# Kernel optimization log

Measured on AMD Instinct MI355X. Metric: run time of the kernel, lower is better.

## Reference

```python
import jax, jax.numpy as jnp
import numpy as np

B, N, D, H = 2, 2048, 1024, 16
Dh = D // H
SCALE = Dh ** -0.5


def setup_inputs() -> dict:
    key = jax.random.key(0)
    ks = jax.random.split(key, 5)
    init = lambda k, sh, fan: (jax.random.normal(k, sh, jnp.float32) / np.sqrt(fan)).astype(jnp.float32)
    return {
        "x": jax.random.normal(ks[0], (B, N, D), jnp.float32),
        "w_qkv": init(ks[1], (D, 3 * D), D),   # to_qkv (no bias)
        "w_hkv": init(ks[2], (D, 2 * D), D),   # hkv_processor: Linear(dim, 2*dim), split -> HK, HV
        "w_out": init(ks[3], (D, D), D),       # to_out weight
        "b_out": jnp.zeros((D,), jnp.float32), # to_out bias
        "alpha": jnp.ones((1, H, 1, 1), jnp.float32),
    }


def _split_heads(t):  # (B,N,D) -> (B,H,N,Dh)
    return t.reshape(B, N, H, Dh).transpose(0, 2, 1, 3)


def _rope(x, theta=10000.0):
    # lucidrains rotary_embedding_torch: interleaved pairs (x[2i], x[2i+1])
    n, dh = x.shape[-2], x.shape[-1]
    freqs = 1.0 / (theta ** (jnp.arange(0, dh, 2, dtype=jnp.float32) / dh))
    ang = jnp.arange(n, dtype=jnp.float32)[:, None] * freqs          # (N, Dh/2)
    cos = jnp.repeat(jnp.cos(ang), 2, axis=-1)                        # (N, Dh)
    sin = jnp.repeat(jnp.sin(ang), 2, axis=-1)
    xp = x.reshape(*x.shape[:-1], dh // 2, 2)
    xrot = jnp.stack((-xp[..., 1], xp[..., 0]), axis=-1).reshape(x.shape)
    return x * cos + xrot * sin


def reference(x, w_qkv, w_hkv, w_out, b_out, alpha):
    q, k, v = (_split_heads(t) for t in jnp.split(x @ w_qkv, 3, axis=-1))
    hk, hv = (_split_heads(t) for t in jnp.split(x @ w_hkv, 2, axis=-1))
    q = _rope(q)
    k = _rope(k)

    qk = jnp.einsum('bhnd,bhmd->bhnm', q, k) * SCALE          # (B,H,N,N)
    hkk = jnp.einsum('bhnd,bhmd->bhnm', hk, k)                # (B,H,N,N)
    qhk = jnp.sum(q * hk, axis=-1, keepdims=True)             # (B,H,N,1)
    scores = qk - jax.nn.silu(hkk * qhk * SCALE)

    mask = jnp.tril(jnp.ones((N, N), dtype=bool))
    scores = jnp.where(mask, scores, -jnp.inf)
    W = jax.nn.softmax(scores, axis=-1)

    hvv = jnp.einsum('bhnd,bhmd->bhnm', hv, v)                # (B,H,N,N)
    mod = jnp.sum(hvv * W, axis=-1, keepdims=True)            # (B,H,N,1)
    o = jnp.einsum('bhnm,bhmd->bhnd', W, v) - jax.nn.sigmoid(alpha) * mod * hv

    attn_out = o.transpose(0, 2, 1, 3).reshape(B, N, D)
    return attn_out @ w_out + b_out
```

## Files before the change

kernel.cpp:

```cpp
#include <hip/hip_runtime.h>
#include <math.h>

typedef unsigned int u32;
typedef unsigned short u16;
typedef __attribute__((ext_vector_type(4))) float f32x4;
typedef __attribute__((ext_vector_type(8))) short s16x8;

#define BB 2
#define NN 2048
#define DD 1024
#define HH 16
#define ROWS 4096
#define QC 5120
#define SCALE 0.125f
#define LOG2E 1.44269504088896f
#define SC2 (SCALE * LOG2E)
#define DEFER_THR 8.0f

#if __has_builtin(__builtin_amdgcn_exp2f)
#define EXP2(x) __builtin_amdgcn_exp2f(x)
#else
#define EXP2(x) __expf((x) * 0.69314718056f)
#endif
#if __has_builtin(__builtin_amdgcn_rcpf)
#define RCP(x) __builtin_amdgcn_rcpf(x)
#else
#define RCP(x) (1.0f / (x))
#endif

__device__ __forceinline__ u16 f2bf(float x) {
    u32 u = __float_as_uint(x);
    return (u16)((u + 0x7FFFu + ((u >> 16) & 1u)) >> 16);
}
__device__ __forceinline__ float bf2f(u16 h) {
    return __uint_as_float(((u32)h) << 16);
}
__device__ __forceinline__ u32 cvtpk(float lo, float hi) {
    u32 r;
    asm("v_cvt_pk_bf16_f32 %0, %1, %2" : "=v"(r) : "v"(lo), "v"(hi));
    return r;
}
__device__ __forceinline__ void gload16(const void* g, void* l) {
    __builtin_amdgcn_global_load_lds(
        (const __attribute__((address_space(1))) unsigned int*)g,
        (__attribute__((address_space(3))) unsigned int*)l, 16, 0, 0);
}

__device__ __forceinline__ void vt_write(char* vbb, uint4 vreg, int srow, int sch)
{
    uint4 oth;
    oth.x = (u32)__shfl_xor((int)vreg.x, 8); oth.y = (u32)__shfl_xor((int)vreg.y, 8);
    oth.z = (u32)__shfl_xor((int)vreg.z, 8); oth.w = (u32)__shfl_xor((int)vreg.w, 8);
    const bool odd = (srow & 1);
    u32 ma = odd ? vreg.z : vreg.x, mb = odd ? vreg.w : vreg.y;
    u32 oa = odd ? oth.z : oth.x,  ob = odd ? oth.w : oth.y;
    u32 ea = odd ? oa : ma, eb = odd ? ob : mb;
    u32 da = odd ? ma : oa, db = odd ? mb : ob;
    u32 pk0 = (ea & 0xffffu) | (da << 16);
    u32 pk1 = (ea >> 16)     | (da & 0xffff0000u);
    u32 pk2 = (eb & 0xffffu) | (db << 16);
    u32 pk3 = (eb >> 16)     | (db & 0xffff0000u);
    const int s = srow >> 1;
    const int d0 = sch * 8 + (odd ? 4 : 0);
    const int sb = (s & 3) * 4;
    *(u32*)(vbb + (d0 + 0) * 128 + ((((s >> 2) ^ ((d0 + 0) & 7) ^ sch) << 4)) + sb) = pk0;
    *(u32*)(vbb + (d0 + 1) * 128 + ((((s >> 2) ^ ((d0 + 1) & 7) ^ sch) << 4)) + sb) = pk1;
    *(u32*)(vbb + (d0 + 2) * 128 + ((((s >> 2) ^ ((d0 + 2) & 7) ^ sch) << 4)) + sb) = pk2;
    *(u32*)(vbb + (d0 + 3) * 128 + ((((s >> 2) ^ ((d0 + 3) & 7) ^ sch) << 4)) + sb) = pk3;
}

__global__ __launch_bounds__(256) void prep(const float* __restrict__ x,
                                            const float* __restrict__ wqkv,
                                            const float* __restrict__ whkv,
                                            const float* __restrict__ wout,
                                            uint4* __restrict__ xb,
                                            u16* __restrict__ wT,
                                            float* __restrict__ tab)
{
    __shared__ float T[64][65];
    const int bid = blockIdx.x;
    if (bid < 2048) {
        int t = bid * 256 + threadIdx.x;
        const float4 a = ((const float4*)x)[2 * t];
        const float4 b = ((const float4*)x)[2 * t + 1];
        uint4 o;
        o.x = f2bf(a.x) | ((u32)f2bf(a.y) << 16);
        o.y = f2bf(a.z) | ((u32)f2bf(a.w) << 16);
        o.z = f2bf(b.x) | ((u32)f2bf(b.y) << 16);
        o.w = f2bf(b.z) | ((u32)f2bf(b.w) << 16);
        xb[t] = o;
    } else if (bid < 3584) {
        const int idx = bid - 2048;
        const int bc = idx % 96;
        const int k0 = (idx / 96) * 64;
        const int c0 = bc * 64;
        const float* src; int stride; int csrc;
        if (bc < 48)      { src = wqkv; stride = 3072; csrc = c0; }
        else if (bc < 80) { src = whkv; stride = 2048; csrc = c0 - 3072; }
        else              { src = wout; stride = 1024; csrc = c0 - 5120; }
        const int t = threadIdx.x;
        const int r = t >> 4, c4 = t & 15;
#pragma unroll
        for (int i = 0; i < 4; ++i) {
            int kk = r + 16 * i;
            float4 v = *(const float4*)&src[(size_t)(k0 + kk) * stride + csrc + 4 * c4];
            T[kk][4 * c4 + 0] = v.x; T[kk][4 * c4 + 1] = v.y;
            T[kk][4 * c4 + 2] = v.z; T[kk][4 * c4 + 3] = v.w;
        }
        __syncthreads();
#pragma unroll
        for (int i = 0; i < 4; ++i) {
            int cc = r + 16 * i;
            u32 lo = f2bf(T[4 * c4 + 0][cc]) | ((u32)f2bf(T[4 * c4 + 1][cc]) << 16);
            u32 hi = f2bf(T[4 * c4 + 2][cc]) | ((u32)f2bf(T[4 * c4 + 3][cc]) << 16);
            *(uint2*)&wT[(size_t)(c0 + cc) * 1024 + k0 + 4 * c4] = make_uint2(lo, hi);
        }
    } else {
        int t = (bid - 3584) * 256 + threadIdx.x;
        int n = t >> 6, col = t & 63, i = col & 31;
        float ang = (float)n * exp2f(-(float)i * 0.41524101186092029f);
        tab[t] = (col < 32) ? cosf(ang) : sinf(ang);
    }
}

template <int BF16_OUT>
__global__ __launch_bounds__(256, 2) void gemm_bf16(
    const u16* __restrict__ A, int lda,
    const u16* __restrict__ B, int ldb,
    void* __restrict__ C, int ldc,
    const float* __restrict__ bias, const float* __restrict__ tab, int K)
{
    __shared__ u16 As[128 * 64];
    __shared__ u16 Bs[128 * 64];
    const int tid = threadIdx.x;
    const int lane = tid & 63, w = tid >> 6;
    const int g = lane >> 4, c = lane & 15;
    const int wr = w >> 1, wc = w & 1;
    const int rb0 = blockIdx.y * 128, cb0 = blockIdx.x * 128;

    f32x4 acc[4][4];
#pragma unroll
    for (int i = 0; i < 4; ++i)
#pragma unroll
        for (int j = 0; j < 4; ++j) {
            acc[i][j][0] = 0.f; acc[i][j][1] = 0.f; acc[i][j][2] = 0.f; acc[i][j][3] = 0.f;
        }

    const int srow = tid >> 3, sch = tid & 7;
    const int scol = ((sch ^ (srow & 7)) * 8);
    const u16* asrc = A + (size_t)(rb0 + srow) * lda + scol;
    const u16* bsrc = B + (size_t)(cb0 + srow) * ldb + scol;

    for (int k0 = 0; k0 < K; k0 += 64) {
        __syncthreads();
#pragma unroll
        for (int r = 0; r < 4; ++r) {
            gload16(asrc + (size_t)(32 * r) * lda + k0, (char*)As + r * 4096 + w * 1024);
            gload16(bsrc + (size_t)(32 * r) * ldb + k0, (char*)Bs + r * 4096 + w * 1024);
        }
        __syncthreads();
#pragma unroll
        for (int kk = 0; kk < 2; ++kk) {
            s16x8 a[4], b[4];
#pragma unroll
            for (int rb = 0; rb < 4; ++rb) {
                int row = wr * 64 + rb * 16 + c;
                a[rb] = *(const s16x8*)((const char*)As + row * 128 + ((((kk << 2) + g) ^ (row & 7)) << 4));
            }
#pragma unroll
            for (int cb = 0; cb < 4; ++cb) {
                int row = wc * 64 + cb * 16 + c;
                b[cb] = *(const s16x8*)((const char*)Bs + row * 128 + ((((kk << 2) + g) ^ (row & 7)) << 4));
            }
#pragma unroll
            for (int rb = 0; rb < 4; ++rb)
#pragma unroll
                for (int cb = 0; cb < 4; ++cb)
                    acc[rb][cb] = __builtin_amdgcn_mfma_f32_16x16x32_bf16(a[rb], b[cb], acc[rb][cb], 0, 0, 0);
        }
    }

    if (BF16_OUT && tab && cb0 >= 1024 && cb0 < 2048) {
#pragma unroll
        for (int rb = 0; rb < 4; ++rb)
#pragma unroll
            for (int cb = 0; cb < 4; ++cb) {
                const int i = ((wc * 64 + cb * 16 + c) & 63) >> 1;
#pragma unroll
                for (int e = 0; e < 4; ++e) {
                    int n = (rb0 + wr * 64 + rb * 16 + g * 4 + e) & (NN - 1);
                    float co = tab[(n << 6) + i], si = tab[(n << 6) + 32 + i];
                    float self = acc[rb][cb][e];
                    float part = __shfl_xor(self, 1);
                    acc[rb][cb][e] = (c & 1) ? fmaf(self, co, part * si)
                                             : fmaf(self, co, -part * si);
                }
            }
    }

#pragma unroll
    for (int rb = 0; rb < 4; ++rb) {
#pragma unroll
        for (int cb = 0; cb < 4; ++cb) {
            if (BF16_OUT) {
                uint2 keep = make_uint2(0, 0);
#pragma unroll
                for (int e = 0; e < 4; ++e) {
                    u32 me = f2bf(acc[rb][cb][e]);
                    u32 x1 = (u32)__shfl_xor((int)me, 1);
                    u32 pair = (c & 1) ? ((x1 & 0xffffu) | (me << 16)) : ((me & 0xffffu) | (x1 << 16));
                    u32 x2 = (u32)__shfl_xor((int)pair, 2);
                    u32 q0 = (c & 2) ? x2 : pair;
                    u32 q1 = (c & 2) ? pair : x2;
                    if ((c & 3) == e) keep = make_uint2(q0, q1);
                }
                int row = rb0 + wr * 64 + rb * 16 + g * 4 + (c & 3);
                int col = cb0 + wc * 64 + cb * 16 + (c & ~3);
                *(uint2*)((u16*)C + (size_t)row * ldc + col) = keep;
            } else {
                int col = cb0 + wc * 64 + cb * 16 + c;
                float bv = bias ? bias[col] : 0.f;
#pragma unroll
                for (int e = 0; e < 4; ++e) {
                    int row = rb0 + wr * 64 + rb * 16 + g * 4 + e;
                    ((float*)C)[(size_t)row * ldc + col] = acc[rb][cb][e] + bv;
                }
            }
        }
    }
}

__global__ __launch_bounds__(256, 4) void attn(
    const u16* __restrict__ qkvh, const float* __restrict__ alpha,
    const float* __restrict__ tab, u16* __restrict__ aout)
{
    __shared__ u16 Kb[2][64 * 64];
    __shared__ u16 Vt[2][64 * 64];

    const int bid = blockIdx.x;
    const int j = bid >> 5;
    const int qt = (j < 8) ? (31 - j) : (j < 16) ? (j + 8) : (j < 24) ? (31 - j) : (j - 24);
    const int bh = 4 * (bid & 7) + ((bid >> 3) & 3);
    const int b = bh >> 4, h = bh & 15;
    const int tid = threadIdx.x;
    const int w = tid >> 6, lane = tid & 63;
    const int g = lane >> 4, c = lane & 15;
    const u16* base = qkvh + (size_t)b * NN * QC;
    const int q0 = qt * 64;
    const int nrow = q0 + w * 16 + c;

    const int srow = tid >> 3, sch = tid & 7;
    const int kscol = (sch ^ ((srow & 3) | (((srow >> 3) & 1) << 2))) * 8;
    const u16* ksrc0 = base + (size_t)srow * QC + 1024 + h * 64 + kscol;
    const u16* vsrc0 = base + (size_t)srow * QC + 2048 + h * 64 + sch * 8;

    const float sig_a = RCP(1.f + EXP2(-alpha[h] * LOG2E));
    const int cbase = (8 * (c >> 2) + (c & 3)) * 128;

    gload16(ksrc0, (char*)&Kb[0][0] + w * 1024);
    gload16(ksrc0 + (size_t)32 * QC, (char*)&Kb[0][0] + 4096 + w * 1024);
    uint4 vr0 = *(const uint4*)vsrc0;
    uint4 vr1 = *(const uint4*)(vsrc0 + (size_t)32 * QC);
    vt_write((char*)&Vt[0][0], vr0, srow, sch);
    vt_write((char*)&Vt[0][0], vr1, srow + 32, sch);

    s16x8 qf[2], hf[2];
    float qhL;
    {
        const u16* qp_ = base + (size_t)nrow * QC + h * 64;
        float accq = 0.f;
#pragma unroll
        for (int kk = 0; kk < 2; ++kk) {
            uint4 qv = *(const uint4*)(qp_ + ((kk * 4 + g) * 8));
            uint4 hv = *(const uint4*)(qp_ + 3072 + ((kk * 4 + g) * 8));
            const u16* qe = (const u16*)&qv;
            const u16* he = (const u16*)&hv;
            u32 ow[4];
#pragma unroll
            for (int m2 = 0; m2 < 4; ++m2) {
                int i = (kk * 4 + g) * 4 + m2;
                float co = tab[(nrow << 6) + i], si = tab[(nrow << 6) + 32 + i];
                float x0 = bf2f(qe[2 * m2]), x1 = bf2f(qe[2 * m2 + 1]);
                float r0 = x0 * co - x1 * si;
                float r1 = x1 * co + x0 * si;
                accq += r0 * bf2f(he[2 * m2]) + r1 * bf2f(he[2 * m2 + 1]);
                ow[m2] = (u32)f2bf(r0) | ((u32)f2bf(r1) << 16);
            }
            union { s16x8 v; u32 u[4]; } uq, uh;
            uq.u[0] = ow[0]; uq.u[1] = ow[1]; uq.u[2] = ow[2]; uq.u[3] = ow[3];
            uh.u[0] = hv.x; uh.u[1] = hv.y; uh.u[2] = hv.z; uh.u[3] = hv.w;
            qf[kk] = uq.v; hf[kk] = uh.v;
        }
        accq += __shfl_xor(accq, 16);
        accq += __shfl_xor(accq, 32);
        qhL = accq * SC2;
    }
    __syncthreads();

    f32x4 y[4];
#pragma unroll
    for (int db = 0; db < 4; ++db) { y[db][0] = 0.f; y[db][1] = 0.f; y[db][2] = 0.f; y[db][3] = 0.f; }
    float m = -INFINITY, l = 0.f;

    for (int kt = 0; kt <= qt; ++kt) {
        const int cur = kt & 1;
        const bool haveNext = (kt < qt);
        uint4 vr0n, vr1n;
        if (haveNext) {
            gload16(ksrc0 + (size_t)((kt + 1) * 64) * QC, (char*)&Kb[cur ^ 1][0] + w * 1024);
            gload16(ksrc0 + (size_t)((kt + 1) * 64 + 32) * QC, (char*)&Kb[cur ^ 1][0] + 4096 + w * 1024);
            vr0n = *(const uint4*)(vsrc0 + (size_t)((kt + 1) * 64) * QC);
            vr1n = *(const uint4*)(vsrc0 + (size_t)((kt + 1) * 64 + 32) * QC);
        }

        f32x4 sq[4], sh4[4];
#pragma unroll
        for (int kb = 0; kb < 4; ++kb) {
            sq[kb][0] = 0.f; sq[kb][1] = 0.f; sq[kb][2] = 0.f; sq[kb][3] = 0.f;
            sh4[kb][0] = 0.f; sh4[kb][1] = 0.f; sh4[kb][2] = 0.f; sh4[kb][3] = 0.f;
        }
        const char* kbp = (const char*)&Kb[cur][0] + cbase;
        __builtin_amdgcn_s_setprio(1);
#pragma unroll
        for (int kb = 0; kb < 4; ++kb) {
#pragma unroll
            for (int kk = 0; kk < 2; ++kk) {
                s16x8 kf = *(const s16x8*)(kbp + (kb & 1) * 512 + (kb >> 1) * 4096 +
                                           ((((kk << 2) + g) ^ (c & 7)) << 4));
                sq[kb] = __builtin_amdgcn_mfma_f32_16x16x32_bf16(kf, qf[kk], sq[kb], 0, 0, 0);
                sh4[kb] = __builtin_amdgcn_mfma_f32_16x16x32_bf16(kf, hf[kk], sh4[kb], 0, 0, 0);
            }
        }
        __builtin_amdgcn_s_setprio(0);
        const bool needmask = (kt == qt);
        float mx = -INFINITY;
#pragma unroll
        for (int kb = 0; kb < 4; ++kb) {
#pragma unroll
            for (int e = 0; e < 4; ++e) {
                float zp = sh4[kb][e] * qhL;
                float sil = zp * RCP(1.f + EXP2(-zp));
                float s = fmaf(sq[kb][e], SC2, -sil);
                if (needmask) {
                    int kg = kt * 64 + 32 * (kb >> 1) + 8 * g + 4 * (kb & 1) + e;
                    if (kg > nrow) s = -INFINITY;
                }
                sq[kb][e] = s;
                mx = fmaxf(mx, s);
            }
        }
        mx = fmaxf(mx, __shfl_xor(mx, 16));
        mx = fmaxf(mx, __shfl_xor(mx, 32));
        if (!__all(mx <= m + DEFER_THR)) {
            const float mnew = fmaxf(m, mx);
            const float scl = EXP2(m - mnew);
            m = mnew;
            l *= scl;
#pragma unroll
            for (int db = 0; db < 4; ++db) {
                y[db][0] *= scl; y[db][1] *= scl; y[db][2] *= scl; y[db][3] *= scl;
            }
        }
        float rs = 0.f;
#pragma unroll
        for (int kb = 0; kb < 4; ++kb)
#pragma unroll
            for (int e = 0; e < 4; ++e) {
                float p = EXP2(sq[kb][e] - m);
                sq[kb][e] = p;
                rs += p;
            }
        rs += __shfl_xor(rs, 16);
        rs += __shfl_xor(rs, 32);
        l += rs;
        union { s16x8 v; u32 u[4]; } pa[2];
#pragma unroll
        for (int kk = 0; kk < 2; ++kk) {
            pa[kk].u[0] = cvtpk(sq[2 * kk][0], sq[2 * kk][1]);
            pa[kk].u[1] = cvtpk(sq[2 * kk][2], sq[2 * kk][3]);
            pa[kk].u[2] = cvtpk(sq[2 * kk + 1][0], sq[2 * kk + 1][1]);
            pa[kk].u[3] = cvtpk(sq[2 * kk + 1][2], sq[2 * kk + 1][3]);
        }
        const char* vbp = (const char*)&Vt[cur][0];
        __builtin_amdgcn_s_setprio(1);
#pragma unroll
        for (int kk = 0; kk < 2; ++kk)
#pragma unroll
            for (int db = 0; db < 4; ++db) {
                int row = db * 16 + c;
                int ch = ((kk << 2) + g) ^ (c & 7) ^ (db * 2 + (c >> 3));
                s16x8 vfr = *(const s16x8*)(vbp + row * 128 + (ch << 4));
                y[db] = __builtin_amdgcn_mfma_f32_16x16x32_bf16(vfr, pa[kk].v, y[db], 0, 0, 0);
            }
        __builtin_amdgcn_s_setprio(0);

        if (haveNext) {
            vt_write((char*)&Vt[cur ^ 1][0], vr0n, srow, sch);
            vt_write((char*)&Vt[cur ^ 1][0], vr1n, srow + 32, sch);
        }
        __syncthreads();
    }

    const float inv_l = RCP(l);
    const u16* hvp = base + (size_t)nrow * QC + 4096 + h * 64 + g * 4;
    float hv[4][4];
    float sdot = 0.f;
#pragma unroll
    for (int db = 0; db < 4; ++db) {
        uint2 hw = *(const uint2*)(hvp + db * 16);
        const u16* he = (const u16*)&hw;
#pragma unroll
        for (int e = 0; e < 4; ++e) {
            hv[db][e] = bf2f(he[e]);
            float yn = y[db][e] * inv_l;
            y[db][e] = yn;
            sdot += yn * hv[db][e];
        }
    }
    sdot += __shfl_xor(sdot, 16);
    sdot += __shfl_xor(sdot, 32);
    const float f = sig_a * sdot;
    u16* op = aout + ((size_t)(b * NN + nrow)) * DD + h * 64 + g * 4;
#pragma unroll
    for (int db = 0; db < 4; ++db) {
        u32 o0 = (u32)f2bf(y[db][0] - f * hv[db][0]) | ((u32)f2bf(y[db][1] - f * hv[db][1]) << 16);
        u32 o1 = (u32)f2bf(y[db][2] - f * hv[db][2]) | ((u32)f2bf(y[db][3] - f * hv[db][3]) << 16);
        *(uint2*)(op + db * 16) = make_uint2(o0, o1);
    }
}

extern "C" void kernel_launch(void* const* d_in, const int* in_sizes, int n_in,
                              void* d_out, int out_size, void* d_ws, size_t ws_size,
                              hipStream_t stream)
{
    const float* x     = (const float*)d_in[0];
    const float* w_qkv = (const float*)d_in[1];
    const float* w_hkv = (const float*)d_in[2];
    const float* w_out = (const float*)d_in[3];
    const float* b_out = (const float*)d_in[4];
    const float* alpha = (const float*)d_in[5];

    char* ws = (char*)d_ws;
    u16*   qkvh = (u16*)ws;
    uint4* xb   = (uint4*)(ws + 41943040);
    u16*   wT   = (u16*)(ws + 50331648);
    u16*   aout = (u16*)(ws + 62914560);
    float* tab  = (float*)(ws + 71303168);

    prep<<<4096, 256, 0, stream>>>(x, w_qkv, w_hkv, w_out, xb, wT, tab);

    gemm_bf16<1><<<dim3(40, 32), 256, 0, stream>>>(
        (const u16*)xb, 1024, wT, 1024, qkvh, QC, nullptr, tab, 1024);

    attn<<<1024, 256, 0, stream>>>(qkvh, alpha, tab, aout);

    gemm_bf16<0><<<dim3(8, 32), 256, 0, stream>>>(
        aout, 1024, wT + 5120 * 1024, 1024, d_out, 1024, b_out, nullptr, 1024);
}
```

Baseline: 159.1 us.

## Use 256x256-tile pipelined GEMM for QKV/HKV projection with 4-stage LDS ring

Result: slower. 174.0 us (+9.4%).

```diff
diff --git a/kernel.cpp b/kernel.cpp
--- a/kernel.cpp
+++ b/kernel.cpp
@@ -123,12 +123,133 @@
     }
 }
 
-template <int BF16_OUT>
-__global__ __launch_bounds__(256, 2) void gemm_bf16(
+__global__ __launch_bounds__(512, 1) void gemm256(
+    const u16* __restrict__ A, const u16* __restrict__ B,
+    u16* __restrict__ C, const float* __restrict__ tab)
+{
+    __shared__ u16 As[4][128 * 64];
+    __shared__ u16 Bs[4][128 * 64];
+    const int tid = threadIdx.x;
+    const int lane = tid & 63, w = tid >> 6;
+    const int g = lane >> 4, c = lane & 15;
+    const int wrow = w >> 2, wcol = w & 3;
+    const int rb0 = blockIdx.y * 256, cb0 = blockIdx.x * 256;
+
+    f32x4 acc[8][4];
+#pragma unroll
+    for (int i = 0; i < 8; ++i)
+#pragma unroll
+        for (int j = 0; j < 4; ++j) {
+            acc[i][j][0] = 0.f; acc[i][j][1] = 0.f; acc[i][j][2] = 0.f; acc[i][j][3] = 0.f;
+        }
+
+    const int srow = tid >> 3, sch = tid & 7;
+    const int scol = (sch ^ (srow & 7)) * 8;
+    const u16* asrc = A + (size_t)(rb0 + srow) * 1024 + scol;
+    const u16* bsrc = B + (size_t)(cb0 + srow) * 1024 + scol;
+
+#define STG(t, h)                                                              \
+    {   const int k_ = (t) * 64;                                               \
+        const int sl_ = (2 * (t) + (h)) & 3;                                   \
+        gload16(asrc + (size_t)((h) * 128) * 1024 + k_,       (char*)As[sl_] + w * 1024);        \
+        gload16(asrc + (size_t)((h) * 128 + 64) * 1024 + k_,  (char*)As[sl_] + 8192 + w * 1024); \
+        gload16(bsrc + (size_t)((h) * 128) * 1024 + k_,       (char*)Bs[sl_] + w * 1024);        \
+        gload16(bsrc + (size_t)((h) * 128 + 64) * 1024 + k_,  (char*)Bs[sl_] + 8192 + w * 1024); \
+    }
+
+#define CLUSTER(rlo, kk)                                                       \
+    __builtin_amdgcn_s_setprio(1);                                             \
+    _Pragma("unroll")                                                          \
+    for (int rb = 0; rb < 4; ++rb)                                             \
+        _Pragma("unroll")                                                      \
+        for (int cb = 0; cb < 4; ++cb)                                         \
+            acc[(rlo) + rb][cb] = __builtin_amdgcn_mfma_f32_16x16x32_bf16(     \
+                af[(rlo) + rb][kk], bf[cb][kk], acc[(rlo) + rb][cb], 0, 0, 0); \
+    __builtin_amdgcn_s_setprio(0);
+
+    STG(0, 0); STG(0, 1); STG(1, 0); STG(1, 1);
+    asm volatile("s_waitcnt vmcnt(8)" ::: "memory");
+    __builtin_amdgcn_s_barrier();
+
+    const int NT = 16;
+    for (int t = 0; t < NT; ++t) {
+        const char* abase = (const char*)As[(2 * t + wrow) & 3];
+        const char* bbase = (const char*)Bs[(2 * t + (wcol >> 1)) & 3];
+        s16x8 af[8][2], bf[4][2];
+#pragma unroll
+        for (int rb = 0; rb < 8; ++rb)
+#pragma unroll
+            for (int kk = 0; kk < 2; ++kk)
+                af[rb][kk] = *(const s16x8*)(abase + (rb * 16 + c) * 128 +
+                                             ((((kk << 2) + g) ^ (c & 7)) << 4));
+#pragma unroll
+        for (int cb = 0; cb < 4; ++cb)
+#pragma unroll
+            for (int kk = 0; kk < 2; ++kk)
+                bf[cb][kk] = *(const s16x8*)(bbase + ((wcol & 1) * 64 + cb * 16 + c) * 128 +
+                                             ((((kk << 2) + g) ^ (c & 7)) << 4));
+        asm volatile("s_waitcnt lgkmcnt(0)" ::: "memory");
+        __builtin_amdgcn_sched_barrier(0);
+        __builtin_amdgcn_s_barrier();
+        __builtin_amdgcn_sched_barrier(0);
+
+        if (t + 2 < NT) STG(t + 2, 0);
+        CLUSTER(0, 0)
+        if (t + 2 < NT) STG(t + 2, 1);
+        CLUSTER(0, 1)
+        CLUSTER(4, 0)
+        CLUSTER(4, 1)
+
+        if (t + 1 < NT) {
+            if (t + 2 < NT) asm volatile("s_waitcnt vmcnt(8)" ::: "memory");
+            else            asm volatile("s_waitcnt vmcnt(0)" ::: "memory");
+            __builtin_amdgcn_s_barrier();
+            __builtin_amdgcn_sched_barrier(0);
+        }
+    }
+#undef STG
+#undef CLUSTER
+
+    const bool doRope = (cb0 >= 1024 && cb0 < 2048);
+#pragma unroll
+    for (int rb = 0; rb < 8; ++rb) {
+#pragma unroll
+        for (int cb = 0; cb < 4; ++cb) {
+            if (doRope) {
+                const int i = ((wcol * 64 + cb * 16 + c) & 63) >> 1;
+#pragma unroll
+                for (int e = 0; e < 4; ++e) {
+                    int n = (rb0 + wrow * 128 + rb * 16 + g * 4 + e) & (NN - 1);
+                    float co = tab[(n << 6) + i], si = tab[(n << 6) + 32 + i];
+                    float self = acc[rb][cb][e];
+                    float part = __shfl_xor(self, 1);
+                    acc[rb][cb][e] = (c & 1) ? fmaf(self, co, part * si)
+                                             : fmaf(self, co, -part * si);
+                }
+            }
+            uint2 keep = make_uint2(0, 0);
+#pragma unroll
+            for (int e = 0; e < 4; ++e) {
+                u32 me = f2bf(acc[rb][cb][e]);
+                u32 x1 = (u32)__shfl_xor((int)me, 1);
+                u32 pair = (c & 1) ? ((x1 & 0xffffu) | (me << 16)) : ((me & 0xffffu) | (x1 << 16));
+                u32 x2 = (u32)__shfl_xor((int)pair, 2);
+                u32 q0 = (c & 2) ? x2 : pair;
+                u32 q1 = (c & 2) ? pair : x2;
+                if ((c & 3) == e) keep = make_uint2(q0, q1);
+            }
+            int row = rb0 + wrow * 128 + rb * 16 + g * 4 + (c & 3);
+            int col = cb0 + wcol * 64 + cb * 16 + (c & ~3);
+            *(uint2*)(C + (size_t)row * QC + col) = keep;
+        }
+    }
+}
+
+__global__ __launch_bounds__(256, 2) void gemm128(
     const u16* __restrict__ A, int lda,
     const u16* __restrict__ B, int ldb,
-    void* __restrict__ C, int ldc,
-    const float* __restrict__ bias, const float* __restrict__ tab, int K)
+    float* __restrict__ C, int ldc,
+    const float* __restrict__ bias, int K)
 {
     __shared__ u16 As[128 * 64];
     __shared__ u16 Bs[128 * 64];
@@ -179,52 +300,16 @@
                     acc[rb][cb] = __builtin_amdgcn_mfma_f32_16x16x32_bf16(a[rb], b[cb], acc[rb][cb], 0, 0, 0);
         }
     }
-
-    if (BF16_OUT && tab && cb0 >= 1024 && cb0 < 2048) {
-#pragma unroll
-        for (int rb = 0; rb < 4; ++rb)
-#pragma unroll
-            for (int cb = 0; cb < 4; ++cb) {
-                const int i = ((wc * 64 + cb * 16 + c) & 63) >> 1;
-#pragma unroll
-                for (int e = 0; e < 4; ++e) {
-                    int n = (rb0 + wr * 64 + rb * 16 + g * 4 + e) & (NN - 1);
-                    float co = tab[(n << 6) + i], si = tab[(n << 6) + 32 + i];
-                    float self = acc[rb][cb][e];
-                    float part = __shfl_xor(self, 1);
-                    acc[rb][cb][e] = (c & 1) ? fmaf(self, co, part * si)
-                                             : fmaf(self, co, -part * si);
-                }
-            }
-    }
-
 #pragma unroll
     for (int rb = 0; rb < 4; ++rb) {
 #pragma unroll
         for (int cb = 0; cb < 4; ++cb) {
-            if (BF16_OUT) {
-                uint2 keep = make_uint2(0, 0);
-#pragma unroll
-                for (int e = 0; e < 4; ++e) {
-                    u32 me = f2bf(acc[rb][cb][e]);
-                    u32 x1 = (u32)__shfl_xor((int)me, 1);
-                    u32 pair = (c & 1) ? ((x1 & 0xffffu) | (me << 16)) : ((me & 0xffffu) | (x1 << 16));
-                    u32 x2 = (u32)__shfl_xor((int)pair, 2);
-                    u32 q0 = (c & 2) ? x2 : pair;
-                    u32 q1 = (c & 2) ? pair : x2;
-                    if ((c & 3) == e) keep = make_uint2(q0, q1);
-                }
-                int row = rb0 + wr * 64 + rb * 16 + g * 4 + (c & 3);
-                int col = cb0 + wc * 64 + cb * 16 + (c & ~3);
-                *(uint2*)((u16*)C + (size_t)row * ldc + col) = keep;
-            } else {
-                int col = cb0 + wc * 64 + cb * 16 + c;
-                float bv = bias ? bias[col] : 0.f;
-#pragma unroll
-                for (int e = 0; e < 4; ++e) {
-                    int row = rb0 + wr * 64 + rb * 16 + g * 4 + e;
-                    ((float*)C)[(size_t)row * ldc + col] = acc[rb][cb][e] + bv;
-                }
+            int col = cb0 + wc * 64 + cb * 16 + c;
+            float bv = bias ? bias[col] : 0.f;
+#pragma unroll
+            for (int e = 0; e < 4; ++e) {
+                int row = rb0 + wr * 64 + rb * 16 + g * 4 + e;
+                C[(size_t)row * ldc + col] = acc[rb][cb][e] + bv;
             }
         }
     }
@@ -449,11 +534,10 @@
 
     prep<<<4096, 256, 0, stream>>>(x, w_qkv, w_hkv, w_out, xb, wT, tab);
 
-    gemm_bf16<1><<<dim3(40, 32), 256, 0, stream>>>(
-        (const u16*)xb, 1024, wT, 1024, qkvh, QC, nullptr, tab, 1024);
+    gemm256<<<dim3(20, 16), 512, 0, stream>>>((const u16*)xb, wT, qkvh, tab);
 
     attn<<<1024, 256, 0, stream>>>(qkvh, alpha, tab, aout);
 
-    gemm_bf16<0><<<dim3(8, 32), 256, 0, stream>>>(
-        aout, 1024, wT + 5120 * 1024, 1024, d_out, 1024, b_out, nullptr, 1024);
-}
+    gemm128<<<dim3(8, 32), 256, 0, stream>>>(
+        aout, 1024, wT + 5120 * 1024, 1024, (float*)d_out, 1024, b_out, 1024);
+}
```
